# Kernel tuning notes

Measured on AMD Instinct MI355X. Metric: run time of the kernel, lower is better.

## Reference

```python
import jax, jax.numpy as jnp
import numpy as np

DIM = 512
HEADS = 8
DIM_HEAD = 64
HIDDEN = HEADS * DIM_HEAD  # 512
B, H, W = 32, 64, 64


def setup_inputs() -> dict:
    key = jax.random.key(0)
    k1, k2, k3 = jax.random.split(key, 3)
    x = jax.random.normal(k1, (B, H, W, DIM), dtype=jnp.float32)
    w_qkv = jax.random.normal(k2, (DIM, 3 * HIDDEN), dtype=jnp.float32) * 0.02
    w_out = jax.random.normal(k3, (HIDDEN, DIM), dtype=jnp.float32) * 0.02
    b_out = jnp.zeros((DIM,), dtype=jnp.float32)
    return {"x": x, "w_qkv": w_qkv, "w_out": w_out, "b_out": b_out}


def reference(x, w_qkv, w_out, b_out):
    b, h, w, c = x.shape
    n = h * w
    scale = DIM_HEAD ** (-0.5)
    # 1x1 conv (no bias) == matmul over channels
    qkv = jnp.einsum('bhwc,cf->bhwf', x, w_qkv)  # (b, h, w, 3*hidden)
    q, k, v = jnp.split(qkv, 3, axis=-1)
    # 'b x y (h c) -> b (x y) h c'
    def to_heads(t):
        return t.reshape(b, n, HEADS, DIM_HEAD)
    q, k, v = map(to_heads, (q, k, v))
    q = q * scale
    # contraction over spatial axis d=(x*y): sim (b, dim_head_i, heads, dim_head_j)
    sim = jnp.einsum('bdhi,bdhj->bihj', q, k)
    sim = sim - jnp.max(sim, axis=-1, keepdims=True)
    attn = jax.nn.softmax(sim, axis=-1)
    out = jnp.einsum('bihj,bdhj->bdhi', attn, v)  # (b, n, heads, dim_head)
    out = out.reshape(b, h, w, HIDDEN)
    # output 1x1 conv with bias
    return jnp.einsum('bhwf,fc->bhwc', out, w_out) + b_out
```

## Files before the change

### kernel.cpp

```cpp
#include <hip/hip_runtime.h>
#include <hip/hip_bf16.h>
#include <stdint.h>

using bf16x8 = __attribute__((ext_vector_type(8))) __bf16;
using s16x8  = __attribute__((ext_vector_type(8))) short;
using f32x4  = __attribute__((ext_vector_type(4))) float;

__device__ __forceinline__ uint16_t f2bf(float f) {
    uint32_t u = __builtin_bit_cast(uint32_t, f);
    u += 0x7fffu + ((u >> 16) & 1u);
    return (uint16_t)(u >> 16);
}
__device__ __forceinline__ float bf2f(uint16_t h) {
    return __builtin_bit_cast(float, (uint32_t)h << 16);
}

__device__ __forceinline__ void async16(uint16_t* lds_dst, const uint16_t* g_src) {
    __builtin_amdgcn_global_load_lds(
        (const __attribute__((address_space(1))) void*)g_src,
        (__attribute__((address_space(3))) void*)lds_dst,
        16, 0, 0);
}

__global__ __launch_bounds__(256, 4)
void xtw_k(const float* __restrict__ x, const float* __restrict__ wqkv,
           const float* __restrict__ wout,
           uint16_t* __restrict__ xb, uint16_t* __restrict__ xT,
           uint16_t* __restrict__ wqTs, uint16_t* __restrict__ wkTcat,
           uint16_t* __restrict__ woutT, uint16_t* __restrict__ wv_rm)
{
    __shared__ uint16_t lt[64 * 68];
    const int tid = threadIdx.x;
    const int bi = blockIdx.x;
    if (bi >= 16384) {
        int sec = (bi - 16384) >> 10;
        int idx = ((bi - 16384) & 1023) * 256 + tid;
        int co = idx >> 9, r = idx & 511;
        if (sec == 0) {
            wqTs[co * 512 + r] = f2bf(wqkv[r * 1536 + co] * 0.125f);
        } else if (sec == 1) {
            uint16_t v = f2bf(wqkv[r * 1536 + 512 + co]);
            wkTcat[co * 1024 + r] = v;
            wkTcat[co * 1024 + 512 + r] = v;
        } else if (sec == 2) {
            woutT[co * 512 + r] = f2bf(wout[r * 512 + co]);
        } else {
            wv_rm[co * 512 + r] = f2bf(wqkv[co * 1536 + 1024 + r]);
        }
        return;
    }
    const int b = bi >> 9;
    const int rem = bi & 511;
    const int st = rem >> 3, ct = rem & 7;
    const int c4 = (tid & 15) * 4;
#pragma unroll
    for (int rep = 0; rep < 4; ++rep) {
        int r = (tid >> 4) + rep * 16;
        long gs = (long)(b * 4096 + st * 64 + r) * 512 + ct * 64 + c4;
        float4 v = *(const float4*)(x + gs);
        uint16_t t[4];
        t[0] = f2bf(v.x); t[1] = f2bf(v.y); t[2] = f2bf(v.z); t[3] = f2bf(v.w);
        *(ushort4*)(xb + gs) = *(const ushort4*)t;
#pragma unroll
        for (int q = 0; q < 4; ++q) lt[r * 68 + c4 + q] = t[q];
    }
    __syncthreads();
    const int s4 = (tid & 15) * 4;
#pragma unroll
    for (int rep = 0; rep < 4; ++rep) {
        int c = (tid >> 4) + rep * 16;
        uint16_t t[4];
#pragma unroll
        for (int q = 0; q < 4; ++q) t[q] = lt[(s4 + q) * 68 + c];
        *(ushort4*)(xT + (long)(b * 512 + ct * 64 + c) * 4096 + st * 64 + s4) =
            *(const ushort4*)t;
    }
}

template<bool OUTF32>
__global__ __launch_bounds__(512, 2)
void g8_k(const uint16_t* __restrict__ A, const uint16_t* __restrict__ Bt,
          void* __restrict__ Cp, const float* __restrict__ bias,
          int K, int lda, int ldb, int ldc, int mtiles, int ntiles,
          long abr, long bbe, long cbr)
{
    __shared__ uint16_t lds[65536];
    const int tid  = threadIdx.x;
    const int lane = tid & 63;
    const int wv   = tid >> 6;
    const int wr   = wv >> 2, wc = wv & 3;

    const int q8 = gridDim.x >> 3;
    const int l  = (blockIdx.x & 7) * q8 + (blockIdx.x >> 3);
    const int per   = mtiles * ntiles;
    const int batch = l / per;
    const int rem   = l - batch * per;
    const int mt    = rem / ntiles, nt = rem - mt * ntiles;

    const long arow0 = abr * batch + (long)mt * 256;
    const uint16_t* abase = A + arow0 * (long)lda;
    const uint16_t* btb   = Bt + bbe * batch + (long)nt * 256 * ldb;

    const int fr = lane & 15;
    const int cx0 = (((0 << 2) | (lane >> 4)) ^ (fr & 7)) * 8;
    const int cx1 = (((1 << 2) | (lane >> 4)) ^ (fr & 7)) * 8;
    const int baseA = wr * 8192 + fr * 64;
    const int baseB = (2 + (wc >> 1)) * 8192 + ((wc & 1) * 64 + fr) * 64;

    const int NT = K >> 6;

    auto stage = [&](int slot, const uint16_t* gb, int rstride, int k0) {
#pragma unroll
        for (int i = 0; i < 2; ++i) {
            int si = i * 512 + wv * 64 + lane;
            int rr = si >> 3, cc = (si & 7) ^ (rr & 7);
            async16(&lds[slot * 8192 + (i * 512 + wv * 64) * 8],
                    gb + (long)rr * rstride + k0 + cc * 8);
        }
    };

    f32x4 acc[8][4];
#pragma unroll
    for (int m = 0; m < 8; ++m)
#pragma unroll
        for (int n = 0; n < 4; ++n) acc[m][n] = (f32x4){0.f, 0.f, 0.f, 0.f};

    bf16x8 af[4], bfq[4];

    auto rdA = [&](int mb, int b4, int cx) {
#pragma unroll
        for (int mi = 0; mi < 4; ++mi)
            af[mi] = __builtin_bit_cast(bf16x8,
                *(const s16x8*)&lds[b4 * 8192 + baseA + (mb + mi) * 1024 + cx]);
    };
    auto rdB = [&](int b4, int cx) {
#pragma unroll
        for (int n = 0; n < 4; ++n)
            bfq[n] = __builtin_bit_cast(bf16x8,
                *(const s16x8*)&lds[b4 * 8192 + baseB + n * 1024 + cx]);
    };
    auto mm = [&](int mb) {
        asm volatile("s_waitcnt lgkmcnt(0)" ::: "memory");
        __builtin_amdgcn_sched_barrier(0);
        __builtin_amdgcn_s_setprio(1);
#pragma unroll
        for (int mi = 0; mi < 4; ++mi)
#pragma unroll
            for (int n = 0; n < 4; ++n)
                acc[mb + mi][n] = __builtin_amdgcn_mfma_f32_16x16x32_bf16(
                    af[mi], bfq[n], acc[mb + mi][n], 0, 0, 0);
        __builtin_amdgcn_s_setprio(0);
        __builtin_amdgcn_s_barrier();
    };

    stage(0, abase,              lda, 0);
    stage(1, abase + 128L * lda, lda, 0);
    stage(2, btb,                ldb, 0);
    stage(3, btb + 128L * ldb,   ldb, 0);
    stage(6, btb,                ldb, 64);
    stage(7, btb + 128L * ldb,   ldb, 64);
    asm volatile("s_waitcnt vmcnt(4)" ::: "memory");
    __builtin_amdgcn_sched_barrier(0);
    __builtin_amdgcn_s_barrier();

    for (int it = 0; it < (NT >> 1); ++it) {
        const int E = 2 * it, Od = E + 1;
        const bool s3 = (E + 2) < NT;
        const bool s7 = (Od + 2) < NT;
        const int kE2 = (E + 2) << 6, kO1 = Od << 6, kO2 = (Od + 2) << 6;

        rdB(0, cx0); rdA(0, 0, cx0);
        stage(4, abase,              lda, kO1);
        stage(5, abase + 128L * lda, lda, kO1);
        __builtin_amdgcn_s_barrier();
        mm(0);
        rdA(4, 0, cx0);
        __builtin_amdgcn_s_barrier();
        mm(4);
        rdB(0, cx1); rdA(0, 0, cx1);
        __builtin_amdgcn_s_barrier();
        mm(0);
        rdA(4, 0, cx1);
        if (s3) {
            stage(2, btb,              ldb, kE2);
            stage(3, btb + 128L * ldb, ldb, kE2);
            asm volatile("s_waitcnt vmcnt(4)" ::: "memory");
        } else {
            asm volatile("s_waitcnt vmcnt(0)" ::: "memory");
        }
        __builtin_amdgcn_sched_barrier(0);
        __builtin_amdgcn_s_barrier();
        mm(4);
        rdB(4, cx0); rdA(0, 4, cx0);
        if (s3) {
            stage(0, abase,              lda, kE2);
            stage(1, abase + 128L * lda, lda, kE2);
        }
        __builtin_amdgcn_s_barrier();
        mm(0);
        rdA(4, 4, cx0);
        __builtin_amdgcn_s_barrier();
        mm(4);
        rdB(4, cx1); rdA(0, 4, cx1);
        __builtin_amdgcn_s_barrier();
        mm(0);
        rdA(4, 4, cx1);
        if (s7) {
            stage(6, btb,              ldb, kO2);
            stage(7, btb + 128L * ldb, ldb, kO2);
            asm volatile("s_waitcnt vmcnt(4)" ::: "memory");
        } else {
            asm volatile("s_waitcnt vmcnt(0)" ::: "memory");
        }
        __builtin_amdgcn_sched_barrier(0);
        __builtin_amdgcn_s_barrier();
        mm(4);
    }

    const long crow0 = cbr * batch + (long)mt * 256 + wr * 128;
    const int  col0  = nt * 256 + wc * 64;
    float bv[4];
#pragma unroll
    for (int n = 0; n < 4; ++n)
        bv[n] = bias ? bias[col0 + n * 16 + (lane & 15)] : 0.f;
#pragma unroll
    for (int m = 0; m < 8; ++m) {
#pragma unroll
        for (int r = 0; r < 4; ++r) {
            long row = crow0 + m * 16 + (lane >> 4) * 4 + r;
#pragma unroll
            for (int n = 0; n < 4; ++n) {
                int col = col0 + n * 16 + (lane & 15);
                float v = acc[m][n][r];
                if constexpr (OUTF32)
                    ((float*)Cp)[row * (long)ldc + col] = v + bv[n];
                else
                    ((uint16_t*)Cp)[row * (long)ldc + col] = f2bf(v);
            }
        }
    }
}

__global__ __launch_bounds__(256, 4)
void g128G_k(const uint16_t* __restrict__ X, uint16_t* __restrict__ Gcat)
{
    __shared__ uint16_t Al[8192];
    __shared__ uint16_t Bl[8192];
    const int tid  = threadIdx.x;
    const int lane = tid & 63;
    const int wv   = tid >> 6;
    const int wr   = wv >> 1, wc = wv & 1;

    const int q8 = gridDim.x >> 3;
    const int l  = (blockIdx.x & 7) * q8 + (blockIdx.x >> 3);
    const int g  = l / 10;
    const int t  = l - g * 10;
    const int i  = (t < 4) ? 0 : ((t < 7) ? 1 : ((t < 9) ? 2 : 3));
    const int j  = t - ((i == 0) ? 0 : (i == 1) ? 3 : (i == 2) ? 5 : 6);
    const int b  = g >> 1, z = g & 1;

    const uint16_t* xz   = X + (long)b * 512 * 4096 + z * 2048;
    const uint16_t* arow = xz + (long)i * 128 * 4096;
    const uint16_t* brow = xz + (long)j * 128 * 4096;

    f32x4 acc[4][4];
#pragma unroll
    for (int m = 0; m < 4; ++m)
#pragma unroll
        for (int n = 0; n < 4; ++n) acc[m][n] = (f32x4){0.f, 0.f, 0.f, 0.f};

    for (int k0 = 0; k0 < 2048; k0 += 64) {
#pragma unroll
        for (int s2 = 0; s2 < 4; ++s2) {
            int cb  = s2 * 256 + wv * 64;
            int ci  = cb + lane;
            int row = ci >> 3;
            int cs  = (ci & 7) ^ (row & 7);
            async16(&Al[cb * 8], arow + (long)row * 4096 + k0 + cs * 8);
            async16(&Bl[cb * 8], brow + (long)row * 4096 + k0 + cs * 8);
        }
        __syncthreads();
#pragma unroll
        for (int ks = 0; ks < 2; ++ks) {
            bf16x8 af[4], bfr[4];
#pragma unroll
            for (int m = 0; m < 4; ++m) {
                int row = wr * 64 + m * 16 + (lane & 15);
                int ch  = ks * 4 + (lane >> 4);
                s16x8 v = *(const s16x8*)&Al[row * 64 + ((ch ^ (row & 7)) * 8)];
                af[m] = __builtin_bit_cast(bf16x8, v);
            }
#pragma unroll
            for (int n = 0; n < 4; ++n) {
                int row = wc * 64 + n * 16 + (lane & 15);
                int ch  = ks * 4 + (lane >> 4);
                s16x8 v = *(const s16x8*)&Bl[row * 64 + ((ch ^ (row & 7)) * 8)];
                bfr[n] = __builtin_bit_cast(bf16x8, v);
            }
#pragma unroll
            for (int m = 0; m < 4; ++m)
#pragma unroll
                for (int n = 0; n < 4; ++n)
                    acc[m][n] = __builtin_amdgcn_mfma_f32_16x16x32_bf16(
                        af[m], bfr[n], acc[m][n], 0, 0, 0);
        }
        __syncthreads();
    }

    uint16_t* o = Gcat + (long)b * 524288;
    const int zoff = z * 512;
    const int row0 = i * 128 + wr * 64;
    const int col0 = j * 128 + wc * 64;
#pragma unroll
    for (int m = 0; m < 4; ++m) {
#pragma unroll
        for (int r = 0; r < 4; ++r) {
            int row = row0 + m * 16 + (lane >> 4) * 4 + r;
#pragma unroll
            for (int n = 0; n < 4; ++n)
                o[(long)row * 1024 + zoff + col0 + n * 16 + (lane & 15)] = f2bf(acc[m][n][r]);
        }
        if (i != j) {
            int rbase = row0 + m * 16 + (lane >> 4) * 4;
#pragma unroll
            for (int n = 0; n < 4; ++n) {
                int col = col0 + n * 16 + (lane & 15);
                uint16_t tt[4];
#pragma unroll
                for (int r = 0; r < 4; ++r) tt[r] = f2bf(acc[m][n][r]);
                *(ushort4*)&o[(long)col * 1024 + zoff + rbase] = *(const ushort4*)tt;
            }
        }
    }
}

__global__ __launch_bounds__(512, 1)
void simfull_k(const uint16_t* __restrict__ Gcat, const uint16_t* __restrict__ wkTcat,
               const uint16_t* __restrict__ wqTs, uint16_t* __restrict__ attn)
{
    __shared__ uint16_t sm[73728];
    const int tid  = threadIdx.x;
    const int lane = tid & 63;
    const int wv   = tid >> 6;
    const int fr   = lane & 15;
    const int hi4  = lane >> 4;
    const int bi = blockIdx.x;
    const int h = bi >> 5;
    const int b = (bi & 7) * 4 + ((bi >> 3) & 3);

    const uint16_t* gb  = Gcat + (long)b * 524288;
    const uint16_t* ab  = wkTcat + (long)h * 64 * 1024;
    const uint16_t* qb2 = wqTs + (long)h * 64 * 512;

    auto stg = [&](int q, int t) {
        const int k0 = t * 32;
#pragma unroll
        for (int i = 0; i < 4; ++i) {
            int si = i * 64 + lane;
            int rr = si >> 2, cc = (si & 3) ^ ((rr >> 1) & 3);
            async16(&sm[q * 16384 + wv * 2048 + i * 512],
                    gb + (long)(wv * 64 + rr) * 1024 + k0 + cc * 8);
        }
        {
            int si = (wv & 3) * 64 + lane;
            int rr = si >> 2, cc = (si & 3) ^ ((rr >> 1) & 3);
            async16(&sm[49152 + q * 4096 + (wv >> 2) * 2048 + (wv & 3) * 512],
                    ab + (long)rr * 1024 + k0 + cc * 8);
        }
    };

    f32x4 acc[4][4];
#pragma unroll
    for (int mf = 0; mf < 4; ++mf)
#pragma unroll
        for (int nf = 0; nf < 4; ++nf) acc[mf][nf] = (f32x4){0.f, 0.f, 0.f, 0.f};

    const int sa = (hi4 ^ ((fr >> 1) & 3)) * 8;

    stg(0, 0);
    stg(1, 1);
    asm volatile("s_waitcnt vmcnt(5)" ::: "memory");
    __builtin_amdgcn_sched_barrier(0);
    __builtin_amdgcn_s_barrier();

    for (int t = 0; t < 32; ++t) {
        const int q = t % 3;
        if (t + 2 < 32) stg((t + 2) % 3, t + 2);
        bf16x8 af[4], bfq[4];
        const int wkb = 49152 + q * 4096 + (wv >> 2) * 2048;
#pragma unroll
        for (int mf = 0; mf < 4; ++mf)
            af[mf] = __builtin_bit_cast(bf16x8,
                *(const s16x8*)&sm[wkb + (mf * 16 + fr) * 32 + sa]);
#pragma unroll
        for (int nf = 0; nf < 4; ++nf)
            bfq[nf] = __builtin_bit_cast(bf16x8,
                *(const s16x8*)&sm[q * 16384 + wv * 2048 + (nf * 16 + fr) * 32 + sa]);
        asm volatile("s_waitcnt lgkmcnt(0)" ::: "memory");
        __builtin_amdgcn_sched_barrier(0);
        __builtin_amdgcn_s_setprio(1);
#pragma unroll
        for (int mf = 0; mf < 4; ++mf)
#pragma unroll
            for (int nf = 0; nf < 4; ++nf)
                acc[mf][nf] = __builtin_amdgcn_mfma_f32_16x16x32_bf16(
                    af[mf], bfq[nf], acc[mf][nf], 0, 0, 0);
        __builtin_amdgcn_s_setprio(0);
        if (t + 2 < 32) { asm volatile("s_waitcnt vmcnt(5)" ::: "memory"); }
        else            { asm volatile("s_waitcnt vmcnt(0)" ::: "memory"); }
        __builtin_amdgcn_sched_barrier(0);
        __builtin_amdgcn_s_barrier();
    }

#pragma unroll
    for (int mf = 0; mf < 4; ++mf)
#pragma unroll
        for (int nf = 0; nf < 4; ++nf)
#pragma unroll
            for (int r = 0; r < 4; ++r) {
                int jj2 = mf * 16 + hi4 * 4 + r;
                int c = wv * 64 + nf * 16 + fr;
                float v = acc[mf][nf][r];
                uint16_t hi = f2bf(v);
                int off = jj2 * 512 + ((c >> 3) ^ (jj2 & 7)) * 8 + (c & 7);
                sm[off] = hi;
                sm[32768 + off] = f2bf(v - bf2f(hi));
            }
    __syncthreads();

    f32x4 a2[4][4];
#pragma unroll
    for (int mf = 0; mf < 4; ++mf)
#pragma unroll
        for (int nf = 0; nf < 4; ++nf) a2[mf][nf] = (f32x4){0.f, 0.f, 0.f, 0.f};
#pragma unroll
    for (int ks = 0; ks < 2; ++ks) {
        bf16x8 af[4], bh[4], bl[4];
#pragma unroll
        for (int mf = 0; mf < 4; ++mf)
            af[mf] = __builtin_bit_cast(bf16x8,
                *(const s16x8*)&qb2[(long)(mf * 16 + fr) * 512 + wv * 64 + ks * 32 + hi4 * 8]);
#pragma unroll
        for (int nf = 0; nf < 4; ++nf) {
            int jj2 = nf * 16 + fr;
            int ch = (wv * 8 + ks * 4 + hi4) ^ (fr & 7);
            bh[nf] = __builtin_bit_cast(bf16x8, *(const s16x8*)&sm[jj2 * 512 + ch * 8]);
            bl[nf] = __builtin_bit_cast(bf16x8, *(const s16x8*)&sm[32768 + jj2 * 512 + ch * 8]);
        }
#pragma unroll
        for (int mf = 0; mf < 4; ++mf)
#pragma unroll
            for (int nf = 0; nf < 4; ++nf) {
                a2[mf][nf] = __builtin_amdgcn_mfma_f32_16x16x32_bf16(
                    af[mf], bh[nf], a2[mf][nf], 0, 0, 0);
                a2[mf][nf] = __builtin_amdgcn_mfma_f32_16x16x32_bf16(
                    af[mf], bl[nf], a2[mf][nf], 0, 0, 0);
            }
    }

    float* red = (float*)&sm[65536];
    for (int w = 0; w < 8; ++w) {
        if (wv == w) {
#pragma unroll
            for (int mf = 0; mf < 4; ++mf)
#pragma unroll
                for (int nf = 0; nf < 4; ++nf)
#pragma unroll
                    for (int r = 0; r < 4; ++r) {
                        int ii = mf * 16 + hi4 * 4 + r;
                        int jj2 = nf * 16 + fr;
                        float* p = &red[ii * 64 + jj2];
                        *p = (w == 0) ? a2[mf][nf][r] : (*p + a2[mf][nf][r]);
                    }
        }
        __syncthreads();
    }

    float* rt1 = (float*)&sm[0];
    float* rt2 = (float*)&sm[512];
    const int ii = tid >> 2, jc = tid & 3;
    float s[16];
    if (tid < 256) {
#pragma unroll
        for (int jj = 0; jj < 16; ++jj) s[jj] = red[ii * 64 + jc * 16 + jj];
        float mx = s[0];
#pragma unroll
        for (int jj = 1; jj < 16; ++jj) mx = fmaxf(mx, s[jj]);
        rt1[ii * 4 + jc] = mx;
    }
    __syncthreads();
    if (tid < 256) {
        float m4 = fmaxf(fmaxf(rt1[ii * 4], rt1[ii * 4 + 1]),
                         fmaxf(rt1[ii * 4 + 2], rt1[ii * 4 + 3]));
        float sum = 0.f;
#pragma unroll
        for (int jj = 0; jj < 16; ++jj) { s[jj] = __expf(s[jj] - m4); sum += s[jj]; }
        rt2[ii * 4 + jc] = sum;
    }
    __syncthreads();
    if (tid < 256) {
        float tot = rt2[ii * 4] + rt2[ii * 4 + 1] + rt2[ii * 4 + 2] + rt2[ii * 4 + 3];
        float inv = 1.f / tot;
        uint16_t* at = attn + (long)(b * 8 + h) * 4096;
#pragma unroll
        for (int jj = 0; jj < 16; ++jj)
            at[ii * 64 + jc * 16 + jj] = f2bf(s[jj] * inv);
    }
}

__global__ __launch_bounds__(512, 1)
void w2v_k(const uint16_t* __restrict__ attn, const uint16_t* __restrict__ woutT,
           const uint16_t* __restrict__ wv_rm, uint16_t* __restrict__ Bteff)
{
    __shared__ uint16_t RT[16384];
    const int tid  = threadIdx.x;
    const int lane = tid & 63;
    const int wv8  = tid >> 6;
    const int wr   = wv8 >> 2, wc = wv8 & 3;
    const int fr   = lane & 15;
    const int hi4  = lane >> 4;

    const int q8 = gridDim.x >> 3;
    const int l  = (blockIdx.x & 7) * q8 + (blockIdx.x >> 3);
    const int b  = l >> 2;
    const int mt = (l >> 1) & 1, nt = l & 1;

    f32x4 acc[8][4];
#pragma unroll
    for (int m = 0; m < 8; ++m)
#pragma unroll
        for (int n = 0; n < 4; ++n) acc[m][n] = (f32x4){0.f, 0.f, 0.f, 0.f};

    for (int h = 0; h < 8; ++h) {
        const uint16_t* ah = attn + (long)(b * 8 + h) * 4096;
        f32x4 rac[4][2];
#pragma unroll
        for (int mf = 0; mf < 4; ++mf)
#pragma unroll
            for (int nf = 0; nf < 2; ++nf) rac[mf][nf] = (f32x4){0.f, 0.f, 0.f, 0.f};
#pragma unroll
        for (int ks = 0; ks < 2; ++ks) {
            bf16x8 af[4], bf2[2];
#pragma unroll
            for (int mf = 0; mf < 4; ++mf)
                af[mf] = __builtin_bit_cast(bf16x8,
                    *(const s16x8*)&ah[(mf * 16 + fr) * 64 + ks * 32 + hi4 * 8]);
#pragma unroll
            for (int nf = 0; nf < 2; ++nf) {
                int k = nt * 256 + wv8 * 32 + nf * 16 + fr;
                bf2[nf] = __builtin_bit_cast(bf16x8,
                    *(const s16x8*)&wv_rm[(long)k * 512 + h * 64 + ks * 32 + hi4 * 8]);
            }
#pragma unroll
            for (int mf = 0; mf < 4; ++mf)
#pragma unroll
                for (int nf = 0; nf < 2; ++nf)
                    rac[mf][nf] = __builtin_amdgcn_mfma_f32_16x16x32_bf16(
                        af[mf], bf2[nf], rac[mf][nf], 0, 0, 0);
        }
        __syncthreads();
#pragma unroll
        for (int mf = 0; mf < 4; ++mf)
#pragma unroll
            for (int nf = 0; nf < 2; ++nf)
#pragma unroll
                for (int r = 0; r < 4; ++r) {
                    int i2 = mf * 16 + hi4 * 4 + r;
                    int k  = wv8 * 32 + nf * 16 + fr;
                    RT[k * 64 + (((i2 >> 3) ^ (k & 7)) * 8) + (i2 & 7)] = f2bf(rac[mf][nf][r]);
                }
        __syncthreads();
#pragma unroll
        for (int ks = 0; ks < 2; ++ks) {
            bf16x8 am[8], bm[4];
#pragma unroll
            for (int mf = 0; mf < 8; ++mf) {
                int c = mt * 256 + wr * 128 + mf * 16 + fr;
                am[mf] = __builtin_bit_cast(bf16x8,
                    *(const s16x8*)&woutT[(long)c * 512 + h * 64 + ks * 32 + hi4 * 8]);
            }
#pragma unroll
            for (int nf = 0; nf < 4; ++nf) {
                int k = wc * 64 + nf * 16 + fr;
                bm[nf] = __builtin_bit_cast(bf16x8,
                    *(const s16x8*)&RT[k * 64 + (((ks * 4 + hi4) ^ (k & 7)) * 8)]);
            }
#pragma unroll
            for (int mf = 0; mf < 8; ++mf)
#pragma unroll
                for (int nf = 0; nf < 4; ++nf)
                    acc[mf][nf] = __builtin_amdgcn_mfma_f32_16x16x32_bf16(
                        am[mf], bm[nf], acc[mf][nf], 0, 0, 0);
        }
    }

    uint16_t* o = Bteff + (long)b * 262144;
#pragma unroll
    for (int mf = 0; mf < 8; ++mf)
#pragma unroll
        for (int r = 0; r < 4; ++r) {
            int c = mt * 256 + wr * 128 + mf * 16 + hi4 * 4 + r;
#pragma unroll
            for (int nf = 0; nf < 4; ++nf) {
                int k = nt * 256 + wc * 64 + nf * 16 + fr;
                o[(long)c * 512 + k] = f2bf(acc[mf][nf][r]);
            }
        }
}

extern "C" void kernel_launch(void* const* d_in, const int* in_sizes, int n_in,
                              void* d_out, int out_size, void* d_ws, size_t ws_size,
                              hipStream_t stream)
{
    const float* x     = (const float*)d_in[0];
    const float* w_qkv = (const float*)d_in[1];
    const float* w_out = (const float*)d_in[2];
    const float* b_out = (const float*)d_in[3];
    float* out = (float*)d_out;

    char* ws = (char*)d_ws;
    uint16_t* xb     = (uint16_t*)(ws);
    uint16_t* xT     = (uint16_t*)(ws + 134217728L);
    uint16_t* Gcat   = (uint16_t*)(ws + 268435456L);
    uint16_t* attn   = (uint16_t*)(ws + 301989888L);
    uint16_t* Bteff  = (uint16_t*)(ws + 320864256L);
    uint16_t* wqTs   = (uint16_t*)(ws + 354418688L);
    uint16_t* wkTcat = (uint16_t*)(ws + 354942976L);
    uint16_t* woutT  = (uint16_t*)(ws + 355991552L);
    uint16_t* wv_rm  = (uint16_t*)(ws + 356515840L);

    xtw_k<<<20480, 256, 0, stream>>>(x, w_qkv, w_out, xb, xT,
                                     wqTs, wkTcat, woutT, wv_rm);

    g128G_k<<<640, 256, 0, stream>>>(xT, Gcat);

    simfull_k<<<256, 512, 0, stream>>>(Gcat, wkTcat, wqTs, attn);

    w2v_k<<<128, 512, 0, stream>>>(attn, woutT, wv_rm, Bteff);

    g8_k<true><<<1024, 512, 0, stream>>>(
        xb, Bteff, out, b_out,
        512, 512, 512, 512, 16, 2, 4096L, 262144L, 4096L);
}
```

Before: 391.8 us.

## Replace split-K Gram matrix with full-K pass and use 128-tile final GEMM

The Gram matrix kernel no longer splits the spatial contraction into two halves written side by side. It now runs the full 4096-length reduction in one pass, which halves the grid and the G buffer. The downstream sim kernel therefore reads a 512-wide G with half the k-steps, and the duplicated wkT concatenation is dropped. The final output GEMM swaps the 256x256 8-wave pipelined kernel for a simpler 128x128 4-wave kernel with 4096 blocks. This trades the hand-tuned software pipelining for more occupancy and more blocks, and the Gram kernel gets less parallelism.

```diff
diff --git a/kernel.cpp b/kernel.cpp
--- a/kernel.cpp
+++ b/kernel.cpp
@@ -26,7 +26,7 @@
 void xtw_k(const float* __restrict__ x, const float* __restrict__ wqkv,
            const float* __restrict__ wout,
            uint16_t* __restrict__ xb, uint16_t* __restrict__ xT,
-           uint16_t* __restrict__ wqTs, uint16_t* __restrict__ wkTcat,
+           uint16_t* __restrict__ wqTs, uint16_t* __restrict__ wkT,
            uint16_t* __restrict__ woutT, uint16_t* __restrict__ wv_rm)
 {
     __shared__ uint16_t lt[64 * 68];
@@ -39,9 +39,7 @@
         if (sec == 0) {
             wqTs[co * 512 + r] = f2bf(wqkv[r * 1536 + co] * 0.125f);
         } else if (sec == 1) {
-            uint16_t v = f2bf(wqkv[r * 1536 + 512 + co]);
-            wkTcat[co * 1024 + r] = v;
-            wkTcat[co * 1024 + 512 + r] = v;
+            wkT[co * 512 + r] = f2bf(wqkv[r * 1536 + 512 + co]);
         } else if (sec == 2) {
             woutT[co * 512 + r] = f2bf(wout[r * 512 + co]);
         } else {
@@ -77,172 +75,8 @@
     }
 }
 
-template<bool OUTF32>
-__global__ __launch_bounds__(512, 2)
-void g8_k(const uint16_t* __restrict__ A, const uint16_t* __restrict__ Bt,
-          void* __restrict__ Cp, const float* __restrict__ bias,
-          int K, int lda, int ldb, int ldc, int mtiles, int ntiles,
-          long abr, long bbe, long cbr)
-{
-    __shared__ uint16_t lds[65536];
-    const int tid  = threadIdx.x;
-    const int lane = tid & 63;
-    const int wv   = tid >> 6;
-    const int wr   = wv >> 2, wc = wv & 3;
-
-    const int q8 = gridDim.x >> 3;
-    const int l  = (blockIdx.x & 7) * q8 + (blockIdx.x >> 3);
-    const int per   = mtiles * ntiles;
-    const int batch = l / per;
-    const int rem   = l - batch * per;
-    const int mt    = rem / ntiles, nt = rem - mt * ntiles;
-
-    const long arow0 = abr * batch + (long)mt * 256;
-    const uint16_t* abase = A + arow0 * (long)lda;
-    const uint16_t* btb   = Bt + bbe * batch + (long)nt * 256 * ldb;
-
-    const int fr = lane & 15;
-    const int cx0 = (((0 << 2) | (lane >> 4)) ^ (fr & 7)) * 8;
-    const int cx1 = (((1 << 2) | (lane >> 4)) ^ (fr & 7)) * 8;
-    const int baseA = wr * 8192 + fr * 64;
-    const int baseB = (2 + (wc >> 1)) * 8192 + ((wc & 1) * 64 + fr) * 64;
-
-    const int NT = K >> 6;
-
-    auto stage = [&](int slot, const uint16_t* gb, int rstride, int k0) {
-#pragma unroll
-        for (int i = 0; i < 2; ++i) {
-            int si = i * 512 + wv * 64 + lane;
-            int rr = si >> 3, cc = (si & 7) ^ (rr & 7);
-            async16(&lds[slot * 8192 + (i * 512 + wv * 64) * 8],
-                    gb + (long)rr * rstride + k0 + cc * 8);
-        }
-    };
-
-    f32x4 acc[8][4];
-#pragma unroll
-    for (int m = 0; m < 8; ++m)
-#pragma unroll
-        for (int n = 0; n < 4; ++n) acc[m][n] = (f32x4){0.f, 0.f, 0.f, 0.f};
-
-    bf16x8 af[4], bfq[4];
-
-    auto rdA = [&](int mb, int b4, int cx) {
-#pragma unroll
-        for (int mi = 0; mi < 4; ++mi)
-            af[mi] = __builtin_bit_cast(bf16x8,
-                *(const s16x8*)&lds[b4 * 8192 + baseA + (mb + mi) * 1024 + cx]);
-    };
-    auto rdB = [&](int b4, int cx) {
-#pragma unroll
-        for (int n = 0; n < 4; ++n)
-            bfq[n] = __builtin_bit_cast(bf16x8,
-                *(const s16x8*)&lds[b4 * 8192 + baseB + n * 1024 + cx]);
-    };
-    auto mm = [&](int mb) {
-        asm volatile("s_waitcnt lgkmcnt(0)" ::: "memory");
-        __builtin_amdgcn_sched_barrier(0);
-        __builtin_amdgcn_s_setprio(1);
-#pragma unroll
-        for (int mi = 0; mi < 4; ++mi)
-#pragma unroll
-            for (int n = 0; n < 4; ++n)
-                acc[mb + mi][n] = __builtin_amdgcn_mfma_f32_16x16x32_bf16(
-                    af[mi], bfq[n], acc[mb + mi][n], 0, 0, 0);
-        __builtin_amdgcn_s_setprio(0);
-        __builtin_amdgcn_s_barrier();
-    };
-
-    stage(0, abase,              lda, 0);
-    stage(1, abase + 128L * lda, lda, 0);
-    stage(2, btb,                ldb, 0);
-    stage(3, btb + 128L * ldb,   ldb, 0);
-    stage(6, btb,                ldb, 64);
-    stage(7, btb + 128L * ldb,   ldb, 64);
-    asm volatile("s_waitcnt vmcnt(4)" ::: "memory");
-    __builtin_amdgcn_sched_barrier(0);
-    __builtin_amdgcn_s_barrier();
-
-    for (int it = 0; it < (NT >> 1); ++it) {
-        const int E = 2 * it, Od = E + 1;
-        const bool s3 = (E + 2) < NT;
-        const bool s7 = (Od + 2) < NT;
-        const int kE2 = (E + 2) << 6, kO1 = Od << 6, kO2 = (Od + 2) << 6;
-
-        rdB(0, cx0); rdA(0, 0, cx0);
-        stage(4, abase,              lda, kO1);
-        stage(5, abase + 128L * lda, lda, kO1);
-        __builtin_amdgcn_s_barrier();
-        mm(0);
-        rdA(4, 0, cx0);
-        __builtin_amdgcn_s_barrier();
-        mm(4);
-        rdB(0, cx1); rdA(0, 0, cx1);
-        __builtin_amdgcn_s_barrier();
-        mm(0);
-        rdA(4, 0, cx1);
-        if (s3) {
-            stage(2, btb,              ldb, kE2);
-            stage(3, btb + 128L * ldb, ldb, kE2);
-            asm volatile("s_waitcnt vmcnt(4)" ::: "memory");
-        } else {
-            asm volatile("s_waitcnt vmcnt(0)" ::: "memory");
-        }
-        __builtin_amdgcn_sched_barrier(0);
-        __builtin_amdgcn_s_barrier();
-        mm(4);
-        rdB(4, cx0); rdA(0, 4, cx0);
-        if (s3) {
-            stage(0, abase,              lda, kE2);
-            stage(1, abase + 128L * lda, lda, kE2);
-        }
-        __builtin_amdgcn_s_barrier();
-        mm(0);
-        rdA(4, 4, cx0);
-        __builtin_amdgcn_s_barrier();
-        mm(4);
-        rdB(4, cx1); rdA(0, 4, cx1);
-        __builtin_amdgcn_s_barrier();
-        mm(0);
-        rdA(4, 4, cx1);
-        if (s7) {
-            stage(6, btb,              ldb, kO2);
-            stage(7, btb + 128L * ldb, ldb, kO2);
-            asm volatile("s_waitcnt vmcnt(4)" ::: "memory");
-        } else {
-            asm volatile("s_waitcnt vmcnt(0)" ::: "memory");
-        }
-        __builtin_amdgcn_sched_barrier(0);
-        __builtin_amdgcn_s_barrier();
-        mm(4);
-    }
-
-    const long crow0 = cbr * batch + (long)mt * 256 + wr * 128;
-    const int  col0  = nt * 256 + wc * 64;
-    float bv[4];
-#pragma unroll
-    for (int n = 0; n < 4; ++n)
-        bv[n] = bias ? bias[col0 + n * 16 + (lane & 15)] : 0.f;
-#pragma unroll
-    for (int m = 0; m < 8; ++m) {
-#pragma unroll
-        for (int r = 0; r < 4; ++r) {
-            long row = crow0 + m * 16 + (lane >> 4) * 4 + r;
-#pragma unroll
-            for (int n = 0; n < 4; ++n) {
-                int col = col0 + n * 16 + (lane & 15);
-                float v = acc[m][n][r];
-                if constexpr (OUTF32)
-                    ((float*)Cp)[row * (long)ldc + col] = v + bv[n];
-                else
-                    ((uint16_t*)Cp)[row * (long)ldc + col] = f2bf(v);
-            }
-        }
-    }
-}
-
 __global__ __launch_bounds__(256, 4)
-void g128G_k(const uint16_t* __restrict__ X, uint16_t* __restrict__ Gcat)
+void g128G_k(const uint16_t* __restrict__ X, uint16_t* __restrict__ G)
 {
     __shared__ uint16_t Al[8192];
     __shared__ uint16_t Bl[8192];
@@ -253,15 +87,14 @@
 
     const int q8 = gridDim.x >> 3;
     const int l  = (blockIdx.x & 7) * q8 + (blockIdx.x >> 3);
-    const int g  = l / 10;
-    const int t  = l - g * 10;
+    const int b  = l / 10;
+    const int t  = l - b * 10;
     const int i  = (t < 4) ? 0 : ((t < 7) ? 1 : ((t < 9) ? 2 : 3));
     const int j  = t - ((i == 0) ? 0 : (i == 1) ? 3 : (i == 2) ? 5 : 6);
-    const int b  = g >> 1, z = g & 1;
-
-    const uint16_t* xz   = X + (long)b * 512 * 4096 + z * 2048;
-    const uint16_t* arow = xz + (long)i * 128 * 4096;
-    const uint16_t* brow = xz + (long)j * 128 * 4096;
+
+    const uint16_t* xbase = X + (long)b * 512 * 4096;
+    const uint16_t* arow  = xbase + (long)i * 128 * 4096;
+    const uint16_t* brow  = xbase + (long)j * 128 * 4096;
 
     f32x4 acc[4][4];
 #pragma unroll
@@ -269,7 +102,7 @@
 #pragma unroll
         for (int n = 0; n < 4; ++n) acc[m][n] = (f32x4){0.f, 0.f, 0.f, 0.f};
 
-    for (int k0 = 0; k0 < 2048; k0 += 64) {
+    for (int k0 = 0; k0 < 4096; k0 += 64) {
 #pragma unroll
         for (int s2 = 0; s2 < 4; ++s2) {
             int cb  = s2 * 256 + wv * 64;
@@ -287,15 +120,15 @@
             for (int m = 0; m < 4; ++m) {
                 int row = wr * 64 + m * 16 + (lane & 15);
                 int ch  = ks * 4 + (lane >> 4);
-                s16x8 v = *(const s16x8*)&Al[row * 64 + ((ch ^ (row & 7)) * 8)];
-                af[m] = __builtin_bit_cast(bf16x8, v);
+                af[m] = __builtin_bit_cast(bf16x8,
+                    *(const s16x8*)&Al[row * 64 + ((ch ^ (row & 7)) * 8)]);
             }
 #pragma unroll
             for (int n = 0; n < 4; ++n) {
                 int row = wc * 64 + n * 16 + (lane & 15);
                 int ch  = ks * 4 + (lane >> 4);
-                s16x8 v = *(const s16x8*)&Bl[row * 64 + ((ch ^ (row & 7)) * 8)];
-                bfr[n] = __builtin_bit_cast(bf16x8, v);
+                bfr[n] = __builtin_bit_cast(bf16x8,
+                    *(const s16x8*)&Bl[row * 64 + ((ch ^ (row & 7)) * 8)]);
             }
 #pragma unroll
             for (int m = 0; m < 4; ++m)
@@ -307,8 +140,7 @@
         __syncthreads();
     }
 
-    uint16_t* o = Gcat + (long)b * 524288;
-    const int zoff = z * 512;
+    uint16_t* o = G + (long)b * 262144;
     const int row0 = i * 128 + wr * 64;
     const int col0 = j * 128 + wc * 64;
 #pragma unroll
@@ -318,7 +150,7 @@
             int row = row0 + m * 16 + (lane >> 4) * 4 + r;
 #pragma unroll
             for (int n = 0; n < 4; ++n)
-                o[(long)row * 1024 + zoff + col0 + n * 16 + (lane & 15)] = f2bf(acc[m][n][r]);
+                o[(long)row * 512 + col0 + n * 16 + (lane & 15)] = f2bf(acc[m][n][r]);
         }
         if (i != j) {
             int rbase = row0 + m * 16 + (lane >> 4) * 4;
@@ -328,14 +160,14 @@
                 uint16_t tt[4];
 #pragma unroll
                 for (int r = 0; r < 4; ++r) tt[r] = f2bf(acc[m][n][r]);
-                *(ushort4*)&o[(long)col * 1024 + zoff + rbase] = *(const ushort4*)tt;
+                *(ushort4*)&o[(long)col * 512 + rbase] = *(const ushort4*)tt;
             }
         }
     }
 }
 
 __global__ __launch_bounds__(512, 1)
-void simfull_k(const uint16_t* __restrict__ Gcat, const uint16_t* __restrict__ wkTcat,
+void simfull_k(const uint16_t* __restrict__ G, const uint16_t* __restrict__ wkT,
                const uint16_t* __restrict__ wqTs, uint16_t* __restrict__ attn)
 {
     __shared__ uint16_t sm[73728];
@@ -348,8 +180,8 @@
     const int h = bi >> 5;
     const int b = (bi & 7) * 4 + ((bi >> 3) & 3);
 
-    const uint16_t* gb  = Gcat + (long)b * 524288;
-    const uint16_t* ab  = wkTcat + (long)h * 64 * 1024;
+    const uint16_t* gb  = G + (long)b * 262144;
+    const uint16_t* ab  = wkT + (long)h * 64 * 512;
     const uint16_t* qb2 = wqTs + (long)h * 64 * 512;
 
     auto stg = [&](int q, int t) {
@@ -359,13 +191,13 @@
             int si = i * 64 + lane;
             int rr = si >> 2, cc = (si & 3) ^ ((rr >> 1) & 3);
             async16(&sm[q * 16384 + wv * 2048 + i * 512],
-                    gb + (long)(wv * 64 + rr) * 1024 + k0 + cc * 8);
+                    gb + (long)(wv * 64 + rr) * 512 + k0 + cc * 8);
         }
         {
             int si = (wv & 3) * 64 + lane;
             int rr = si >> 2, cc = (si & 3) ^ ((rr >> 1) & 3);
             async16(&sm[49152 + q * 4096 + (wv >> 2) * 2048 + (wv & 3) * 512],
-                    ab + (long)rr * 1024 + k0 + cc * 8);
+                    ab + (long)rr * 512 + k0 + cc * 8);
         }
     };
 
@@ -383,9 +215,9 @@
     __builtin_amdgcn_sched_barrier(0);
     __builtin_amdgcn_s_barrier();
 
-    for (int t = 0; t < 32; ++t) {
+    for (int t = 0; t < 16; ++t) {
         const int q = t % 3;
-        if (t + 2 < 32) stg((t + 2) % 3, t + 2);
+        if (t + 2 < 16) stg((t + 2) % 3, t + 2);
         bf16x8 af[4], bfq[4];
         const int wkb = 49152 + q * 4096 + (wv >> 2) * 2048;
 #pragma unroll
@@ -406,7 +238,7 @@
                 acc[mf][nf] = __builtin_amdgcn_mfma_f32_16x16x32_bf16(
                     af[mf], bfq[nf], acc[mf][nf], 0, 0, 0);
         __builtin_amdgcn_s_setprio(0);
-        if (t + 2 < 32) { asm volatile("s_waitcnt vmcnt(5)" ::: "memory"); }
+        if (t + 2 < 16) { asm volatile("s_waitcnt vmcnt(5)" ::: "memory"); }
         else            { asm volatile("s_waitcnt vmcnt(0)" ::: "memory"); }
         __builtin_amdgcn_sched_barrier(0);
         __builtin_amdgcn_s_barrier();
@@ -608,6 +440,89 @@
         }
 }
 
+__global__ __launch_bounds__(256, 4)
+void g128_k(const uint16_t* __restrict__ A, const uint16_t* __restrict__ Bt,
+            float* __restrict__ C, const float* __restrict__ bias,
+            int mtiles, int ntiles)
+{
+    __shared__ uint16_t Al[8192];
+    __shared__ uint16_t Bl[8192];
+    const int tid  = threadIdx.x;
+    const int lane = tid & 63;
+    const int wv   = tid >> 6;
+    const int wr   = wv >> 1, wc = wv & 1;
+
+    const int q8 = gridDim.x >> 3;
+    const int l  = (blockIdx.x & 7) * q8 + (blockIdx.x >> 3);
+    const int per   = mtiles * ntiles;
+    const int batch = l / per;
+    const int rem   = l - batch * per;
+    const int mt    = rem / ntiles, nt = rem - mt * ntiles;
+
+    const uint16_t* arow = A + ((long)batch * 4096 + mt * 128) * 512;
+    const uint16_t* brow = Bt + (long)batch * 262144 + (long)nt * 128 * 512;
+
+    f32x4 acc[4][4];
+#pragma unroll
+    for (int m = 0; m < 4; ++m)
+#pragma unroll
+        for (int n = 0; n < 4; ++n) acc[m][n] = (f32x4){0.f, 0.f, 0.f, 0.f};
+
+    for (int k0 = 0; k0 < 512; k0 += 64) {
+#pragma unroll
+        for (int s2 = 0; s2 < 4; ++s2) {
+            int cb  = s2 * 256 + wv * 64;
+            int ci  = cb + lane;
+            int row = ci >> 3;
+            int cs  = (ci & 7) ^ (row & 7);
+            async16(&Al[cb * 8], arow + (long)row * 512 + k0 + cs * 8);
+            async16(&Bl[cb * 8], brow + (long)row * 512 + k0 + cs * 8);
+        }
+        __syncthreads();
+#pragma unroll
+        for (int ks = 0; ks < 2; ++ks) {
+            bf16x8 af[4], bfr[4];
+#pragma unroll
+            for (int m = 0; m < 4; ++m) {
+                int row = wr * 64 + m * 16 + (lane & 15);
+                int ch  = ks * 4 + (lane >> 4);
+                af[m] = __builtin_bit_cast(bf16x8,
+                    *(const s16x8*)&Al[row * 64 + ((ch ^ (row & 7)) * 8)]);
+            }
+#pragma unroll
+            for (int n = 0; n < 4; ++n) {
+                int row = wc * 64 + n * 16 + (lane & 15);
+                int ch  = ks * 4 + (lane >> 4);
+                bfr[n] = __builtin_bit_cast(bf16x8,
+                    *(const s16x8*)&Bl[row * 64 + ((ch ^ (row & 7)) * 8)]);
+            }
+#pragma unroll
+            for (int m = 0; m < 4; ++m)
+#pragma unroll
+                for (int n = 0; n < 4; ++n)
+                    acc[m][n] = __builtin_amdgcn_mfma_f32_16x16x32_bf16(
+                        af[m], bfr[n], acc[m][n], 0, 0, 0);
+        }
+        __syncthreads();
+    }
+
+    const long crow0 = (long)batch * 4096 + mt * 128 + wr * 64;
+    const int  col0  = nt * 128 + wc * 64;
+    float bv[4];
+#pragma unroll
+    for (int n = 0; n < 4; ++n)
+        bv[n] = bias[col0 + n * 16 + (lane & 15)];
+#pragma unroll
+    for (int m = 0; m < 4; ++m)
+#pragma unroll
+        for (int r = 0; r < 4; ++r) {
+            long row = crow0 + m * 16 + (lane >> 4) * 4 + r;
+#pragma unroll
+            for (int n = 0; n < 4; ++n)
+                C[row * 512 + col0 + n * 16 + (lane & 15)] = acc[m][n][r] + bv[n];
+        }
+}
+
 extern "C" void kernel_launch(void* const* d_in, const int* in_sizes, int n_in,
                               void* d_out, int out_size, void* d_ws, size_t ws_size,
                               hipStream_t stream)
@@ -619,26 +534,24 @@
     float* out = (float*)d_out;
 
     char* ws = (char*)d_ws;
-    uint16_t* xb     = (uint16_t*)(ws);
-    uint16_t* xT     = (uint16_t*)(ws + 134217728L);
-    uint16_t* Gcat   = (uint16_t*)(ws + 268435456L);
-    uint16_t* attn   = (uint16_t*)(ws + 301989888L);
-    uint16_t* Bteff  = (uint16_t*)(ws + 320864256L);
-    uint16_t* wqTs   = (uint16_t*)(ws + 354418688L);
-    uint16_t* wkTcat = (uint16_t*)(ws + 354942976L);
-    uint16_t* woutT  = (uint16_t*)(ws + 355991552L);
-    uint16_t* wv_rm  = (uint16_t*)(ws + 356515840L);
+    uint16_t* xb    = (uint16_t*)(ws);
+    uint16_t* xT    = (uint16_t*)(ws + 134217728L);
+    uint16_t* G     = (uint16_t*)(ws + 268435456L);
+    uint16_t* attn  = (uint16_t*)(ws + 285212672L);
+    uint16_t* Bteff = (uint16_t*)(ws + 287309824L);
+    uint16_t* wqTs  = (uint16_t*)(ws + 304087040L);
+    uint16_t* wkT   = (uint16_t*)(ws + 304611328L);
+    uint16_t* woutT = (uint16_t*)(ws + 305135616L);
+    uint16_t* wv_rm = (uint16_t*)(ws + 305659904L);
 
     xtw_k<<<20480, 256, 0, stream>>>(x, w_qkv, w_out, xb, xT,
-                                     wqTs, wkTcat, woutT, wv_rm);
-
-    g128G_k<<<640, 256, 0, stream>>>(xT, Gcat);
-
-    simfull_k<<<256, 512, 0, stream>>>(Gcat, wkTcat, wqTs, attn);
+                                     wqTs, wkT, woutT, wv_rm);
+
+    g128G_k<<<320, 256, 0, stream>>>(xT, G);
+
+    simfull_k<<<256, 512, 0, stream>>>(G, wkT, wqTs, attn);
 
     w2v_k<<<128, 512, 0, stream>>>(attn, woutT, wv_rm, Bteff);
 
-    g8_k<true><<<1024, 512, 0, stream>>>(
-        xb, Bteff, out, b_out,
-        512, 512, 512, 512, 16, 2, 4096L, 262144L, 4096L);
-}
+    g128_k<<<4096, 256, 0, stream>>>(xb, Bteff, out, b_out, 32, 4);
+}
```

Result: slower. 401.9 us (+2.6%).
